# Performance work log

Measured on AMD Instinct MI355X. Metric: run time of the kernel, lower is better.

## Reference

```python
import jax, jax.numpy as jnp
import numpy as np

N = 8192
VOCAB = 32768
EMB = 128
HID = [128, 128]
NUM_CLASSES = 16
NUM_GRAPHS = 64


def setup_inputs() -> dict:
    key = jax.random.key(0)
    ks = jax.random.split(key, 10)
    x = jax.random.randint(ks[0], (N,), 0, VOCAB, dtype=jnp.int64 if jax.config.jax_enable_x64 else jnp.int32)
    m = jax.random.uniform(ks[1], (N, N), dtype=jnp.float32)  # dense weighted adjacency, positive degrees
    bm = (jnp.arange(N) * NUM_GRAPHS) // N  # sorted graph ids, every segment non-empty
    emb = jax.random.normal(ks[2], (VOCAB, EMB), dtype=jnp.float32)
    s1 = 1.0 / np.sqrt(EMB)
    w1 = jax.random.uniform(ks[3], (HID[0], EMB), jnp.float32, -s1, s1)
    b1 = jax.random.uniform(ks[4], (HID[0],), jnp.float32, -s1, s1)
    s2 = 1.0 / np.sqrt(HID[0])
    w2 = jax.random.uniform(ks[5], (HID[1], HID[0]), jnp.float32, -s2, s2)
    b2 = jax.random.uniform(ks[6], (HID[1],), jnp.float32, -s2, s2)
    sc = 1.0 / np.sqrt(HID[1])
    wc = jax.random.uniform(ks[7], (NUM_CLASSES, HID[1]), jnp.float32, -sc, sc)
    bc = jax.random.uniform(ks[8], (NUM_CLASSES,), jnp.float32, -sc, sc)
    return {"x": x, "m": m, "bm": bm, "emb": emb, "w1": w1, "b1": b1,
            "w2": w2, "b2": b2, "wc": wc, "bc": bc}


def _gcn_layer(h, m, w, b):
    # Linear -> ReLU (dropout=0 is identity)
    msg = jax.nn.relu(h @ w.T + b)
    row_deg = jnp.sum(m, axis=1, keepdims=True)   # (N,1)
    col_deg = jnp.sum(m, axis=0, keepdims=True)   # (1,N)
    deg = jnp.sqrt(row_deg) * jnp.sqrt(col_deg)   # rank-1 outer, same as mm(sqrt(rd), sqrt(cd))
    return (m / deg) @ msg                        # (N, out_dim)


def reference(x, m, bm, emb, w1, b1, w2, b2, wc, bc):
    h = emb[x]                                    # (N, EMB) embedding lookup
    h = _gcn_layer(h, m, w1, b1)
    h = _gcn_layer(h, m, w2, b2)
    pooled = jax.ops.segment_max(h, bm, num_segments=NUM_GRAPHS)  # (G, HID[-1]) max-pool per graph
    logits = pooled @ wc.T + bc                   # (G, NUM_CLASSES)
    return logits
```

## Files before the change

### kernel.cpp

```cpp
#include <hip/hip_runtime.h>
#include <stdint.h>


#define NN 8192
#define DH 128
#define NCLS 16
#define NGRAPH 64
#define SPLITK 8
#define KCHUNK (NN / SPLITK)
#define CDSLICE 256

typedef float floatx4 __attribute__((ext_vector_type(4)));
typedef __bf16 bf16x8 __attribute__((ext_vector_type(8)));

__device__ __forceinline__ unsigned f2bf_bits(float f) {
    union { float f; unsigned u; } v; v.f = f;
    unsigned u = v.u;
    u += 0x7fffu + ((u >> 16) & 1u);
    return u >> 16;
}
__device__ __forceinline__ float bf2f(unsigned bits16) {
    union { unsigned u; float f; } v; v.u = bits16 << 16; return v.f;
}

__global__ __launch_bounds__(256) void k_cast(
    const float* __restrict__ m, unsigned short* __restrict__ mb,
    float* __restrict__ rd)
{
    int wv = threadIdx.x >> 6, lane = threadIdx.x & 63;
    int row = blockIdx.x * 4 + wv;
    const float* src = m + (size_t)row * NN;
    unsigned short* dst = mb + (size_t)row * NN;
    float rsum = 0.f;
#pragma unroll 4
    for (int it = 0; it < 32; ++it) {
        int c = it * 256 + lane * 4;
        float4 a = *(const float4*)(src + c);
        rsum += (a.x + a.y) + (a.z + a.w);
        uint2 o;
        o.x = f2bf_bits(a.x) | (f2bf_bits(a.y) << 16);
        o.y = f2bf_bits(a.z) | (f2bf_bits(a.w) << 16);
        *(uint2*)(dst + c) = o;
    }
#pragma unroll
    for (int off = 1; off < 64; off <<= 1) rsum += __shfl_xor(rsum, off, 64);
    if (lane == 0) rd[row] = rsum;
}

__global__ __launch_bounds__(256) void k_cd(
    const unsigned short* __restrict__ mb, float* __restrict__ cdpart)
{
    int cb = blockIdx.x & 3, rb = blockIdx.x >> 2;
    int c = cb * 2048 + threadIdx.x * 8;
    const unsigned short* p = mb + (size_t)rb * 32 * NN + c;
    float s[8];
#pragma unroll
    for (int u = 0; u < 8; ++u) s[u] = 0.f;
#pragma unroll 4
    for (int r = 0; r < 32; ++r) {
        uint4 v = *(const uint4*)(p + (size_t)r * NN);
        s[0] += bf2f(v.x & 0xffffu); s[1] += bf2f(v.x >> 16);
        s[2] += bf2f(v.y & 0xffffu); s[3] += bf2f(v.y >> 16);
        s[4] += bf2f(v.z & 0xffffu); s[5] += bf2f(v.z >> 16);
        s[6] += bf2f(v.w & 0xffffu); s[7] += bf2f(v.w >> 16);
    }
    float* op = cdpart + (size_t)rb * NN + c;
    *(float4*)op = (float4){s[0], s[1], s[2], s[3]};
    *(float4*)(op + 4) = (float4){s[4], s[5], s[6], s[7]};
}

__global__ __launch_bounds__(256) void k_cd2(
    const float* __restrict__ cdpart, float* __restrict__ cd)
{
    int col = blockIdx.x * 256 + threadIdx.x;
    float s = 0.f;
#pragma unroll 8
    for (int r = 0; r < CDSLICE; ++r) s += cdpart[(size_t)r * NN + col];
    cd[col] = s;
}

__global__ __launch_bounds__(256) void k_msg(
    const int* __restrict__ x, const float* __restrict__ emb,
    const float* __restrict__ part, const float* __restrict__ rdv,
    const float* __restrict__ w, const float* __restrict__ bias,
    const float* __restrict__ cdv, unsigned short* __restrict__ msgT,
    int layer)
{
    int tid = threadIdx.x;
    int wv = tid >> 6, lane = tid & 63;
    int quad = lane >> 4, r16 = lane & 15;
    int j = blockIdx.x * 64 + wv * 16 + r16;

    floatx4 acc[8];
#pragma unroll
    for (int t = 0; t < 8; ++t) acc[t] = (floatx4)0.f;

    const float* src;
    float presc = 1.f;
    if (layer == 1) {
        src = emb + (size_t)x[j] * DH;
    } else {
        src = part + (size_t)j * DH;
        presc = rsqrtf(rdv[j]);
    }

#pragma unroll
    for (int e0 = 0; e0 < DH; e0 += 32) {
        int ke = e0 + quad * 8;
        float v[8];
        if (layer == 1) {
            float4 a = *(const float4*)(src + ke);
            float4 b = *(const float4*)(src + ke + 4);
            v[0] = a.x; v[1] = a.y; v[2] = a.z; v[3] = a.w;
            v[4] = b.x; v[5] = b.y; v[6] = b.z; v[7] = b.w;
        } else {
#pragma unroll
            for (int u = 0; u < 8; ++u) v[u] = 0.f;
#pragma unroll
            for (int p2 = 0; p2 < SPLITK; ++p2) {
                const float* pp = src + (size_t)p2 * ((size_t)NN * DH) + ke;
                float4 a = *(const float4*)pp;
                float4 b = *(const float4*)(pp + 4);
                v[0] += a.x; v[1] += a.y; v[2] += a.z; v[3] += a.w;
                v[4] += b.x; v[5] += b.y; v[6] += b.z; v[7] += b.w;
            }
#pragma unroll
            for (int u = 0; u < 8; ++u) v[u] *= presc;
        }
        bf16x8 bf;
#pragma unroll
        for (int u = 0; u < 8; ++u) bf[u] = (__bf16)v[u];
#pragma unroll
        for (int t = 0; t < 8; ++t) {
            const float* wp = w + (size_t)(t * 16 + r16) * DH + ke;
            float4 wa = *(const float4*)wp;
            float4 wb = *(const float4*)(wp + 4);
            bf16x8 af;
            af[0] = (__bf16)wa.x; af[1] = (__bf16)wa.y; af[2] = (__bf16)wa.z; af[3] = (__bf16)wa.w;
            af[4] = (__bf16)wb.x; af[5] = (__bf16)wb.y; af[6] = (__bf16)wb.z; af[7] = (__bf16)wb.w;
            acc[t] = __builtin_amdgcn_mfma_f32_16x16x32_bf16(af, bf, acc[t], 0, 0, 0);
        }
    }
    float cs = rsqrtf(cdv[j]);
#pragma unroll
    for (int t = 0; t < 8; ++t) {
#pragma unroll
        for (int r = 0; r < 4; ++r) {
            int n = t * 16 + quad * 4 + r;
            float val = acc[t][r] + bias[n];
            val = fmaxf(val, 0.f) * cs;
            msgT[(size_t)n * NN + j] = (unsigned short)f2bf_bits(val);
        }
    }
}

__global__ __launch_bounds__(256) void k_gemm(
    const unsigned short* __restrict__ A,
    const unsigned short* __restrict__ Bt,
    float* __restrict__ part)
{
    int mblk = blockIdx.x & 63;
    int kp = blockIdx.x >> 6;
    int tid = threadIdx.x;
    int wv = tid >> 6, lane = tid & 63;
    int quad = lane >> 4, r16 = lane & 15;
    int wm = wv >> 1, wn = wv & 1;
    size_t mbase = (size_t)mblk * 128;
    int kbase = kp * KCHUNK;

    const unsigned short* a0 = A + (mbase + wm * 64 + r16) * (size_t)NN + kbase + quad * 8;
    const unsigned short* b0 = Bt + (size_t)(wn * 64 + r16) * NN + kbase + quad * 8;

    floatx4 acc[4][4];
#pragma unroll
    for (int mi = 0; mi < 4; ++mi)
#pragma unroll
        for (int ni = 0; ni < 4; ++ni) acc[mi][ni] = (floatx4)0.f;

#define LOADF(AB, ks)                                                              \
    do {                                                                           \
        _Pragma("unroll")                                                          \
        for (int q = 0; q < 4; ++q) {                                              \
            AB##a[q] = *(const bf16x8*)(a0 + (size_t)q * 16 * NN + (ks) * 32);     \
            AB##b[q] = *(const bf16x8*)(b0 + (size_t)q * 16 * NN + (ks) * 32);     \
        }                                                                          \
    } while (0)
#define MFMAF(AB)                                                                  \
    do {                                                                           \
        _Pragma("unroll")                                                          \
        for (int mi = 0; mi < 4; ++mi)                                             \
            _Pragma("unroll")                                                      \
            for (int ni = 0; ni < 4; ++ni)                                         \
                acc[mi][ni] = __builtin_amdgcn_mfma_f32_16x16x32_bf16(             \
                    AB##a[mi], AB##b[ni], acc[mi][ni], 0, 0, 0);                   \
    } while (0)

    bf16x8 pa[4], pb[4], qa[4], qb[4];
    LOADF(p, 0);
#pragma unroll
    for (int ks = 0; ks < KCHUNK / 32; ks += 2) {
        LOADF(q, ks + 1);
        MFMAF(p);
        if (ks + 2 < KCHUNK / 32) LOADF(p, ks + 2);
        MFMAF(q);
    }
#undef LOADF
#undef MFMAF

    float* outp = part + (size_t)kp * ((size_t)NN * DH);
#pragma unroll
    for (int mi = 0; mi < 4; ++mi) {
#pragma unroll
        for (int r = 0; r < 4; ++r) {
            size_t i = mbase + wm * 64 + mi * 16 + quad * 4 + r;
            float* op = outp + i * DH + wn * 64 + r16;
#pragma unroll
            for (int ni = 0; ni < 4; ++ni) op[ni * 16] = acc[mi][ni][r];
        }
    }
}

__global__ __launch_bounds__(256) void k_pool(
    const float* __restrict__ part, const float* __restrict__ rdv,
    float* __restrict__ pmax)
{
    __shared__ float red[256];
    int g = blockIdx.x >> 3, rc = blockIdx.x & 7;
    int c = threadIdx.x & 127, rh = threadIdx.x >> 7;
    float mx = -1e30f;
#pragma unroll
    for (int r = 0; r < 8; ++r) {
        int i = g * 128 + rc * 16 + rh * 8 + r;
        float s = 0.f;
#pragma unroll
        for (int p = 0; p < SPLITK; ++p)
            s += part[(size_t)p * ((size_t)NN * DH) + (size_t)i * DH + c];
        mx = fmaxf(mx, s * rsqrtf(rdv[i]));
    }
    red[threadIdx.x] = mx;
    __syncthreads();
    if (rh == 0) pmax[(size_t)(g * 8 + rc) * 128 + c] = fmaxf(red[c], red[c + 128]);
}

__global__ __launch_bounds__(128) void k_classify(
    const float* __restrict__ pmax, const float* __restrict__ wc,
    const float* __restrict__ bc, float* __restrict__ out)
{
    __shared__ float pooled[128];
    int g = blockIdx.x, t = threadIdx.x;
    float mx = pmax[(size_t)(g * 8) * 128 + t];
#pragma unroll
    for (int rc = 1; rc < 8; ++rc)
        mx = fmaxf(mx, pmax[(size_t)(g * 8 + rc) * 128 + t]);
    pooled[t] = mx;
    __syncthreads();
    if (t < NCLS) {
        float a = bc[t];
        const float* wr = wc + t * 128;
#pragma unroll 8
        for (int k = 0; k < 128; ++k) a += pooled[k] * wr[k];
        out[g * NCLS + t] = a;
    }
}

extern "C" void kernel_launch(void* const* d_in, const int* in_sizes, int n_in,
                              void* d_out, int out_size, void* d_ws, size_t ws_size,
                              hipStream_t stream)
{
    const int*   x   = (const int*)  d_in[0];
    const float* m   = (const float*)d_in[1];
    const float* emb = (const float*)d_in[3];
    const float* w1  = (const float*)d_in[4];
    const float* b1  = (const float*)d_in[5];
    const float* w2  = (const float*)d_in[6];
    const float* b2  = (const float*)d_in[7];
    const float* wc  = (const float*)d_in[8];
    const float* bc  = (const float*)d_in[9];
    float* out = (float*)d_out;

    char* ws = (char*)d_ws;
    unsigned short* mb = (unsigned short*)ws;
    float* rd   = (float*)(ws + (size_t)134217728);
    float* cd   = rd + NN;
    unsigned short* msgT = (unsigned short*)(cd + NN);
    float* part = (float*)((char*)msgT + (size_t)2 * NN * DH);
    float* cdpart = part;
    float* pmax = part + (size_t)SPLITK * NN * DH;

    k_cast<<<NN / 4, 256, 0, stream>>>(m, mb, rd);
    k_cd<<<1024, 256, 0, stream>>>(mb, cdpart);
    k_cd2<<<NN / 256, 256, 0, stream>>>(cdpart, cd);
    k_msg<<<NN / 64, 256, 0, stream>>>(x, emb, nullptr, nullptr, w1, b1, cd, msgT, 1);
    k_gemm<<<64 * SPLITK, 256, 0, stream>>>(mb, msgT, part);
    k_msg<<<NN / 64, 256, 0, stream>>>(nullptr, nullptr, part, rd, w2, b2, cd, msgT, 2);
    k_gemm<<<64 * SPLITK, 256, 0, stream>>>(mb, msgT, part);
    k_pool<<<NGRAPH * 8, 256, 0, stream>>>(part, rd, pmax);
    k_classify<<<NGRAPH, 128, 0, stream>>>(pmax, wc, bc, out);
}
```

Baseline: 594.8 us.

## Stage GEMM tiles in LDS via global_load_lds and shrink k_msg blocks

```diff
diff --git a/kernel.cpp b/kernel.cpp
--- a/kernel.cpp
+++ b/kernel.cpp
@@ -21,6 +21,12 @@
 }
 __device__ __forceinline__ float bf2f(unsigned bits16) {
     union { unsigned u; float f; } v; v.u = bits16 << 16; return v.f;
+}
+
+__device__ __forceinline__ void gload16(const void* g, void* l) {
+    __builtin_amdgcn_global_load_lds(
+        (const __attribute__((address_space(1))) void*)g,
+        (__attribute__((address_space(3))) void*)l, 16, 0, 0);
 }
 
 __global__ __launch_bounds__(256) void k_cast(
@@ -79,17 +85,16 @@
     cd[col] = s;
 }
 
-__global__ __launch_bounds__(256) void k_msg(
+__global__ __launch_bounds__(64) void k_msg(
     const int* __restrict__ x, const float* __restrict__ emb,
     const float* __restrict__ part, const float* __restrict__ rdv,
     const float* __restrict__ w, const float* __restrict__ bias,
     const float* __restrict__ cdv, unsigned short* __restrict__ msgT,
     int layer)
 {
-    int tid = threadIdx.x;
-    int wv = tid >> 6, lane = tid & 63;
+    int lane = threadIdx.x & 63;
     int quad = lane >> 4, r16 = lane & 15;
-    int j = blockIdx.x * 64 + wv * 16 + r16;
+    int j = blockIdx.x * 16 + r16;
 
     floatx4 acc[8];
 #pragma unroll
@@ -159,6 +164,8 @@
     const unsigned short* __restrict__ Bt,
     float* __restrict__ part)
 {
+    __shared__ unsigned short lA[128 * 32];
+    __shared__ unsigned short lB[128 * 32];
     int mblk = blockIdx.x & 63;
     int kp = blockIdx.x >> 6;
     int tid = threadIdx.x;
@@ -168,44 +175,40 @@
     size_t mbase = (size_t)mblk * 128;
     int kbase = kp * KCHUNK;
 
-    const unsigned short* a0 = A + (mbase + wm * 64 + r16) * (size_t)NN + kbase + quad * 8;
-    const unsigned short* b0 = Bt + (size_t)(wn * 64 + r16) * NN + kbase + quad * 8;
-
     floatx4 acc[4][4];
 #pragma unroll
     for (int mi = 0; mi < 4; ++mi)
 #pragma unroll
         for (int ni = 0; ni < 4; ++ni) acc[mi][ni] = (floatx4)0.f;
 
-#define LOADF(AB, ks)                                                              \
-    do {                                                                           \
-        _Pragma("unroll")                                                          \
-        for (int q = 0; q < 4; ++q) {                                              \
-            AB##a[q] = *(const bf16x8*)(a0 + (size_t)q * 16 * NN + (ks) * 32);     \
-            AB##b[q] = *(const bf16x8*)(b0 + (size_t)q * 16 * NN + (ks) * 32);     \
-        }                                                                          \
-    } while (0)
-#define MFMAF(AB)                                                                  \
-    do {                                                                           \
-        _Pragma("unroll")                                                          \
-        for (int mi = 0; mi < 4; ++mi)                                             \
-            _Pragma("unroll")                                                      \
-            for (int ni = 0; ni < 4; ++ni)                                         \
-                acc[mi][ni] = __builtin_amdgcn_mfma_f32_16x16x32_bf16(             \
-                    AB##a[mi], AB##b[ni], acc[mi][ni], 0, 0, 0);                   \
-    } while (0)
-
-    bf16x8 pa[4], pb[4], qa[4], qb[4];
-    LOADF(p, 0);
-#pragma unroll
-    for (int ks = 0; ks < KCHUNK / 32; ks += 2) {
-        LOADF(q, ks + 1);
-        MFMAF(p);
-        if (ks + 2 < KCHUNK / 32) LOADF(p, ks + 2);
-        MFMAF(q);
-    }
-#undef LOADF
-#undef MFMAF
+    int srow = lane >> 2;
+    int kq = lane & 3;
+    const unsigned short* gA = A + (mbase + wv * 32 + srow) * (size_t)NN + kbase + kq * 8;
+    const unsigned short* gB = Bt + (size_t)(wv * 32 + srow) * NN + kbase + kq * 8;
+    char* lAw = (char*)lA + wv * 2048;
+    char* lBw = (char*)lB + wv * 2048;
+
+    for (int it = 0; it < KCHUNK / 32; ++it) {
+        gload16(gA, lAw);
+        gload16(gA + (size_t)16 * NN, lAw + 1024);
+        gload16(gB, lBw);
+        gload16(gB + (size_t)16 * NN, lBw + 1024);
+        __syncthreads();
+        bf16x8 af[4], bf[4];
+#pragma unroll
+        for (int mi = 0; mi < 4; ++mi)
+            af[mi] = *(const bf16x8*)((const char*)lA + ((wm * 64 + mi * 16 + r16) * 64 + quad * 16));
+#pragma unroll
+        for (int ni = 0; ni < 4; ++ni)
+            bf[ni] = *(const bf16x8*)((const char*)lB + ((wn * 64 + ni * 16 + r16) * 64 + quad * 16));
+#pragma unroll
+        for (int mi = 0; mi < 4; ++mi)
+#pragma unroll
+            for (int ni = 0; ni < 4; ++ni)
+                acc[mi][ni] = __builtin_amdgcn_mfma_f32_16x16x32_bf16(af[mi], bf[ni], acc[mi][ni], 0, 0, 0);
+        __syncthreads();
+        gA += 32; gB += 32;
+    }
 
     float* outp = part + (size_t)kp * ((size_t)NN * DH);
 #pragma unroll
@@ -290,9 +293,9 @@
     k_cast<<<NN / 4, 256, 0, stream>>>(m, mb, rd);
     k_cd<<<1024, 256, 0, stream>>>(mb, cdpart);
     k_cd2<<<NN / 256, 256, 0, stream>>>(cdpart, cd);
-    k_msg<<<NN / 64, 256, 0, stream>>>(x, emb, nullptr, nullptr, w1, b1, cd, msgT, 1);
+    k_msg<<<NN / 16, 64, 0, stream>>>(x, emb, nullptr, nullptr, w1, b1, cd, msgT, 1);
     k_gemm<<<64 * SPLITK, 256, 0, stream>>>(mb, msgT, part);
-    k_msg<<<NN / 64, 256, 0, stream>>>(nullptr, nullptr, part, rd, w2, b2, cd, msgT, 2);
+    k_msg<<<NN / 16, 64, 0, stream>>>(nullptr, nullptr, part, rd, w2, b2, cd, msgT, 2);
     k_gemm<<<64 * SPLITK, 256, 0, stream>>>(mb, msgT, part);
     k_pool<<<NGRAPH * 8, 256, 0, stream>>>(part, rd, pmax);
     k_classify<<<NGRAPH, 128, 0, stream>>>(pmax, wc, bc, out);
```

Result: faster. 538.5 us (-9.5%).
